# Optimization experiments

Measured on AMD Instinct MI355X. Metric: run time of the kernel, lower is better.

The kernel has to match this reference:

```python
import jax, jax.numpy as jnp
import numpy as np

D_MODEL = 512
NUM_HEADS = 8
D_K = D_MODEL // NUM_HEADS


def setup_inputs() -> dict:
    key = jax.random.key(0)
    ks = jax.random.split(key, 11)
    B, S = 2, 4096
    std = max(0.02, min((1.0 / D_MODEL) ** 0.5, 0.5))
    xavier = (6.0 / (D_MODEL + D_MODEL)) ** 0.5
    return {
        "Q": jax.random.normal(ks[0], (B, S, D_MODEL), jnp.float32),
        "K": jax.random.normal(ks[1], (B, S, D_MODEL), jnp.float32),
        "V": jax.random.normal(ks[2], (B, S, D_MODEL), jnp.float32),
        # torch Linear convention: weight [out, in], y = x @ W.T + b
        "Wq": std * jax.random.truncated_normal(ks[3], -2.0, 2.0, (D_MODEL, D_MODEL), jnp.float32),
        "bq": jnp.zeros((D_MODEL,), jnp.float32),
        "Wk": std * jax.random.truncated_normal(ks[4], -2.0, 2.0, (D_MODEL, D_MODEL), jnp.float32),
        "bk": jnp.zeros((D_MODEL,), jnp.float32),
        "Wv": std * jax.random.truncated_normal(ks[5], -2.0, 2.0, (D_MODEL, D_MODEL), jnp.float32),
        "bv": jnp.zeros((D_MODEL,), jnp.float32),
        "Wo": jax.random.uniform(ks[6], (D_MODEL, D_MODEL), jnp.float32, -xavier, xavier),
        "bo": jnp.zeros((D_MODEL,), jnp.float32),
    }


def _split_heads(x):
    B, S, _ = x.shape
    return x.reshape(B, S, NUM_HEADS, D_K).transpose(0, 2, 1, 3)  # [B,H,S,dk]


def reference(Q, K, V, Wq, bq, Wk, bk, Wv, bv, Wo, bo):
    B, S, _ = Q.shape
    q = _split_heads(Q @ Wq.T + bq)
    k = _split_heads(K @ Wk.T + bk)
    v = _split_heads(V @ Wv.T + bv)
    scores = jnp.einsum("bhqd,bhkd->bhqk", q, k) / (D_K ** 0.5)  # [B,H,S,S]
    causal = jnp.tril(jnp.ones((S, S), bool))  # mask=True path
    scores = jnp.where(causal[None, None], scores, jnp.float32(-1e9))
    attn = jax.nn.softmax(scores, axis=-1)
    out = jnp.einsum("bhqk,bhkd->bhqd", attn, v)
    out = out.transpose(0, 2, 1, 3).reshape(B, S, D_MODEL)
    return out @ Wo.T + bo, attn
```

## Files before the change

kernel.cpp:

```cpp
#include <hip/hip_runtime.h>
#include <stdint.h>

#define B_  2
#define H_  8
#define S_  4096
#define DM_ 512
#define DK_ 64
#define BH_ (B_*H_)

using f32x4 = __attribute__((ext_vector_type(4))) float;
using s16x8 = __attribute__((ext_vector_type(8))) short;
using u16x4 = __attribute__((ext_vector_type(4))) unsigned short;
using u16x8 = __attribute__((ext_vector_type(8))) unsigned short;

__device__ __forceinline__ unsigned short f2bf(float f) {
    unsigned int u = __float_as_uint(f);
    u += 0x7FFFu + ((u >> 16) & 1u);
    return (unsigned short)(u >> 16);
}
__device__ __forceinline__ float bf2f(unsigned short h) {
    return __uint_as_float(((unsigned int)h) << 16);
}

__global__ __launch_bounds__(256) void convert_split(const float* __restrict__ in,
        unsigned short* __restrict__ hi, unsigned short* __restrict__ lo, int n4)
{
    for (int i = blockIdx.x*256 + threadIdx.x; i < n4; i += gridDim.x*256) {
        float4 v = ((const float4*)in)[i];
        float s4[4] = {v.x, v.y, v.z, v.w};
        u16x4 h, l;
#pragma unroll
        for (int j = 0; j < 4; ++j) {
            unsigned short hh = f2bf(s4[j]);
            h[j] = hh; l[j] = f2bf(s4[j] - bf2f(hh));
        }
        ((u16x4*)hi)[i] = h;
        ((u16x4*)lo)[i] = l;
    }
}

__global__ __launch_bounds__(256) void convert_hi(const float* __restrict__ in,
        unsigned short* __restrict__ hi, int n4)
{
    for (int i = blockIdx.x*256 + threadIdx.x; i < n4; i += gridDim.x*256) {
        float4 v = ((const float4*)in)[i];
        u16x4 h;
        h[0] = f2bf(v.x); h[1] = f2bf(v.y); h[2] = f2bf(v.z); h[3] = f2bf(v.w);
        ((u16x4*)hi)[i] = h;
    }
}

template<int MODE>
__global__ __launch_bounds__(256) void proj_kernel(
        const unsigned short* __restrict__ Xh, const unsigned short* __restrict__ Xl,
        const unsigned short* __restrict__ Wh, const unsigned short* __restrict__ Wl,
        const float* __restrict__ bias, unsigned short* __restrict__ Y, float scale)
{
    __shared__ __align__(16) unsigned short xh[64*72], xl[64*72];
    __shared__ __align__(16) unsigned short wh[64*72], wl[64*72];
    const int tid  = threadIdx.x;
    const int wave = tid >> 6, lane = tid & 63, lq = lane >> 4, lr = lane & 15;
    const int m0 = blockIdx.x * 64, n0 = blockIdx.y * 64;

    f32x4 acc[4] = {{0.f,0.f,0.f,0.f},{0.f,0.f,0.f,0.f},
                    {0.f,0.f,0.f,0.f},{0.f,0.f,0.f,0.f}};

    for (int kk = 0; kk < 8; ++kk) {
        __syncthreads();
#pragma unroll
        for (int p = 0; p < 2; ++p) {
            int idx = tid + p*256;
            int row = idx >> 3, seg = idx & 7;
            size_t xoff = (size_t)(m0+row)*DM_ + kk*64 + seg*8;
            size_t woff = (size_t)(n0+row)*DM_ + kk*64 + seg*8;
            *(u16x8*)&xh[row*72 + seg*8] = *(const u16x8*)&Xh[xoff];
            *(u16x8*)&xl[row*72 + seg*8] = *(const u16x8*)&Xl[xoff];
            *(u16x8*)&wh[row*72 + seg*8] = *(const u16x8*)&Wh[woff];
            *(u16x8*)&wl[row*72 + seg*8] = *(const u16x8*)&Wl[woff];
        }
        __syncthreads();
        const int ar = wave*16 + lr;
        s16x8 ah0 = *(const s16x8*)&xh[ar*72 +  0 + lq*8];
        s16x8 ah1 = *(const s16x8*)&xh[ar*72 + 32 + lq*8];
        s16x8 al0 = *(const s16x8*)&xl[ar*72 +  0 + lq*8];
        s16x8 al1 = *(const s16x8*)&xl[ar*72 + 32 + lq*8];
#pragma unroll
        for (int nt = 0; nt < 4; ++nt) {
            int br = nt*16 + lr;
            s16x8 bh0 = *(const s16x8*)&wh[br*72 +  0 + lq*8];
            s16x8 bh1 = *(const s16x8*)&wh[br*72 + 32 + lq*8];
            s16x8 bl0 = *(const s16x8*)&wl[br*72 +  0 + lq*8];
            s16x8 bl1 = *(const s16x8*)&wl[br*72 + 32 + lq*8];
            acc[nt] = __builtin_amdgcn_mfma_f32_16x16x32_bf16(ah0, bh0, acc[nt], 0, 0, 0);
            acc[nt] = __builtin_amdgcn_mfma_f32_16x16x32_bf16(ah0, bl0, acc[nt], 0, 0, 0);
            acc[nt] = __builtin_amdgcn_mfma_f32_16x16x32_bf16(al0, bh0, acc[nt], 0, 0, 0);
            acc[nt] = __builtin_amdgcn_mfma_f32_16x16x32_bf16(ah1, bh1, acc[nt], 0, 0, 0);
            acc[nt] = __builtin_amdgcn_mfma_f32_16x16x32_bf16(ah1, bl1, acc[nt], 0, 0, 0);
            acc[nt] = __builtin_amdgcn_mfma_f32_16x16x32_bf16(al1, bh1, acc[nt], 0, 0, 0);
        }
    }
#pragma unroll
    for (int nt = 0; nt < 4; ++nt)
#pragma unroll
        for (int r = 0; r < 4; ++r) {
            int m = m0 + wave*16 + lq*4 + r;
            int n = n0 + nt*16 + lr;
            float v = (acc[nt][r] + bias[n]) * scale;
            int b = m >> 12, s = m & 4095;
            int h = n >> 6,  d = n & 63;
            size_t addr;
            if (MODE == 0) addr = ((size_t)((b*H_ + h)*S_ + s))*DK_ + d;
            else           addr = ((size_t)((b*H_ + h)*DK_ + d))*S_ + s;
            Y[addr] = f2bf(v);
        }
}

__global__ __launch_bounds__(256) void stats_kernel(
        const unsigned short* __restrict__ qb, const unsigned short* __restrict__ kb,
        float* __restrict__ lsum)
{
    __shared__ __align__(16) unsigned short qs[64*72], ks[64*72];
    const int tid  = threadIdx.x;
    const int wave = tid >> 6, lane = tid & 63, lq = lane >> 4, lr = lane & 15;
    const int bh = blockIdx.y;
    const int s0 = blockIdx.x * 64;

#pragma unroll
    for (int p = 0; p < 2; ++p) {
        int idx = tid + p*256;
        int row = idx >> 3, seg = idx & 7;
        *(s16x8*)&qs[row*72 + seg*8] =
            *(const s16x8*)&qb[((size_t)bh*S_ + s0 + row)*DK_ + seg*8];
    }
    __syncthreads();
    const int ar = wave*16 + lr;
    s16x8 aq0 = *(const s16x8*)&qs[ar*72 +  0 + lq*8];
    s16x8 aq1 = *(const s16x8*)&qs[ar*72 + 32 + lq*8];

    float lacc[4] = {0.f, 0.f, 0.f, 0.f};
    const int jtmax = blockIdx.x;
    for (int jt = 0; jt <= jtmax; ++jt) {
        __syncthreads();
#pragma unroll
        for (int p = 0; p < 2; ++p) {
            int idx = tid + p*256;
            int row = idx >> 3, seg = idx & 7;
            *(s16x8*)&ks[row*72 + seg*8] =
                *(const s16x8*)&kb[((size_t)bh*S_ + jt*64 + row)*DK_ + seg*8];
        }
        __syncthreads();
#pragma unroll
        for (int nt = 0; nt < 4; ++nt) {
            int br = nt*16 + lr;
            s16x8 b0 = *(const s16x8*)&ks[br*72 +  0 + lq*8];
            s16x8 b1 = *(const s16x8*)&ks[br*72 + 32 + lq*8];
            f32x4 sc = {0.f,0.f,0.f,0.f};
            sc = __builtin_amdgcn_mfma_f32_16x16x32_bf16(aq0, b0, sc, 0, 0, 0);
            sc = __builtin_amdgcn_mfma_f32_16x16x32_bf16(aq1, b1, sc, 0, 0, 0);
            int j = jt*64 + nt*16 + lr;
#pragma unroll
            for (int r = 0; r < 4; ++r) {
                int sq = s0 + wave*16 + lq*4 + r;
                lacc[r] += (j <= sq) ? __expf(sc[r] - 16.f) : 0.f;
            }
        }
    }
#pragma unroll
    for (int r = 0; r < 4; ++r) {
        float v = lacc[r];
        for (int off = 1; off < 16; off <<= 1) v += __shfl_xor(v, off, 64);
        if (lr == 0) lsum[(size_t)bh*S_ + s0 + wave*16 + lq*4 + r] = v;
    }
}

__global__ __launch_bounds__(256) void attn_kernel(
        const unsigned short* __restrict__ qb, const unsigned short* __restrict__ kb,
        const unsigned short* __restrict__ vtb, const float* __restrict__ lsum,
        float* __restrict__ attn, unsigned short* __restrict__ oacc)
{
    __shared__ __align__(16) unsigned short qs[64*72], ks[64*72], vs[64*72];
    __shared__ __align__(16) unsigned short ps[4][16*72];
    __shared__ float invl[64];
    const int tid  = threadIdx.x;
    const int wave = tid >> 6, lane = tid & 63, lq = lane >> 4, lr = lane & 15;
    const int bh = blockIdx.y;
    const int s0 = blockIdx.x * 64;

#pragma unroll
    for (int p = 0; p < 2; ++p) {
        int idx = tid + p*256;
        int row = idx >> 3, seg = idx & 7;
        *(s16x8*)&qs[row*72 + seg*8] =
            *(const s16x8*)&qb[((size_t)bh*S_ + s0 + row)*DK_ + seg*8];
    }
    if (tid < 64) invl[tid] = 1.0f / lsum[(size_t)bh*S_ + s0 + tid];
    __syncthreads();
    const int ar = wave*16 + lr;
    s16x8 aq0 = *(const s16x8*)&qs[ar*72 +  0 + lq*8];
    s16x8 aq1 = *(const s16x8*)&qs[ar*72 + 32 + lq*8];
    float il[4];
#pragma unroll
    for (int r = 0; r < 4; ++r) il[r] = invl[wave*16 + lq*4 + r];

    f32x4 O[4] = {{0.f,0.f,0.f,0.f},{0.f,0.f,0.f,0.f},
                  {0.f,0.f,0.f,0.f},{0.f,0.f,0.f,0.f}};
    const int jtcomp = blockIdx.x;

    for (int jt = 0; jt < S_/64; ++jt) {
        if (jt <= jtcomp) {
            __syncthreads();
#pragma unroll
            for (int p = 0; p < 2; ++p) {
                int idx = tid + p*256;
                int row = idx >> 3, seg = idx & 7;
                *(s16x8*)&ks[row*72 + seg*8] =
                    *(const s16x8*)&kb[((size_t)bh*S_ + jt*64 + row)*DK_ + seg*8];
                *(s16x8*)&vs[row*72 + seg*8] =
                    *(const s16x8*)&vtb[((size_t)bh*DK_ + row)*S_ + jt*64 + seg*8];
            }
            __syncthreads();
            float a_all[4][4];
#pragma unroll
            for (int nt = 0; nt < 4; ++nt) {
                int br = nt*16 + lr;
                s16x8 b0 = *(const s16x8*)&ks[br*72 +  0 + lq*8];
                s16x8 b1 = *(const s16x8*)&ks[br*72 + 32 + lq*8];
                f32x4 sc = {0.f,0.f,0.f,0.f};
                sc = __builtin_amdgcn_mfma_f32_16x16x32_bf16(aq0, b0, sc, 0, 0, 0);
                sc = __builtin_amdgcn_mfma_f32_16x16x32_bf16(aq1, b1, sc, 0, 0, 0);
                int j = jt*64 + nt*16 + lr;
#pragma unroll
                for (int r = 0; r < 4; ++r) {
                    int sq = s0 + wave*16 + lq*4 + r;
                    float p = (j <= sq) ? __expf(sc[r] - 16.f) : 0.f;
                    float a = p * il[r];
                    a_all[nt][r] = a;
                    ps[wave][(lq*4 + r)*72 + nt*16 + lr] = f2bf(a);
                }
            }
            asm volatile("s_waitcnt lgkmcnt(0)" ::: "memory");
            __builtin_amdgcn_sched_barrier(0);
            s16x8 ap0 = *(const s16x8*)&ps[wave][lr*72 +  0 + lq*8];
            s16x8 ap1 = *(const s16x8*)&ps[wave][lr*72 + 32 + lq*8];
#pragma unroll
            for (int nt = 0; nt < 4; ++nt) {
                s16x8 bv0 = *(const s16x8*)&vs[(nt*16 + lr)*72 +  0 + lq*8];
                s16x8 bv1 = *(const s16x8*)&vs[(nt*16 + lr)*72 + 32 + lq*8];
                O[nt] = __builtin_amdgcn_mfma_f32_16x16x32_bf16(ap0, bv0, O[nt], 0, 0, 0);
                O[nt] = __builtin_amdgcn_mfma_f32_16x16x32_bf16(ap1, bv1, O[nt], 0, 0, 0);
            }
#pragma unroll
            for (int nt = 0; nt < 4; ++nt)
#pragma unroll
                for (int r = 0; r < 4; ++r) {
                    int sq = s0 + wave*16 + lq*4 + r;
                    attn[((size_t)bh*S_ + sq)*S_ + jt*64 + nt*16 + lr] = a_all[nt][r];
                }
        } else {
#pragma unroll
            for (int p = 0; p < 4; ++p) {
                int idx = tid + p*256;
                int row = idx >> 4, c4 = idx & 15;
                float4 z = {0.f, 0.f, 0.f, 0.f};
                *(float4*)&attn[((size_t)bh*S_ + s0 + row)*S_ + jt*64 + c4*4] = z;
            }
        }
    }
    const int b = bh >> 3, h = bh & 7;
#pragma unroll
    for (int nt = 0; nt < 4; ++nt)
#pragma unroll
        for (int r = 0; r < 4; ++r) {
            int s = s0 + wave*16 + lq*4 + r;
            oacc[((size_t)(b*S_ + s))*DM_ + h*DK_ + nt*16 + lr] = f2bf(O[nt][r]);
        }
}

__global__ __launch_bounds__(256) void outproj_kernel(
        const unsigned short* __restrict__ Xin, const unsigned short* __restrict__ Woh,
        const float* __restrict__ bias, float* __restrict__ out)
{
    __shared__ __align__(16) unsigned short xs[64*72], wsm[64*72];
    const int tid  = threadIdx.x;
    const int wave = tid >> 6, lane = tid & 63, lq = lane >> 4, lr = lane & 15;
    const int m0 = blockIdx.x * 64, n0 = blockIdx.y * 64;

    f32x4 acc[4] = {{0.f,0.f,0.f,0.f},{0.f,0.f,0.f,0.f},
                    {0.f,0.f,0.f,0.f},{0.f,0.f,0.f,0.f}};

    for (int kk = 0; kk < 8; ++kk) {
        __syncthreads();
#pragma unroll
        for (int p = 0; p < 2; ++p) {
            int idx = tid + p*256;
            int row = idx >> 3, seg = idx & 7;
            *(s16x8*)&xs [row*72 + seg*8] =
                *(const s16x8*)&Xin[(size_t)(m0+row)*DM_ + kk*64 + seg*8];
            *(s16x8*)&wsm[row*72 + seg*8] =
                *(const s16x8*)&Woh[(size_t)(n0+row)*DM_ + kk*64 + seg*8];
        }
        __syncthreads();
        const int ar = wave*16 + lr;
        s16x8 a0 = *(const s16x8*)&xs[ar*72 +  0 + lq*8];
        s16x8 a1 = *(const s16x8*)&xs[ar*72 + 32 + lq*8];
#pragma unroll
        for (int nt = 0; nt < 4; ++nt) {
            int br = nt*16 + lr;
            s16x8 b0 = *(const s16x8*)&wsm[br*72 +  0 + lq*8];
            s16x8 b1 = *(const s16x8*)&wsm[br*72 + 32 + lq*8];
            acc[nt] = __builtin_amdgcn_mfma_f32_16x16x32_bf16(a0, b0, acc[nt], 0, 0, 0);
            acc[nt] = __builtin_amdgcn_mfma_f32_16x16x32_bf16(a1, b1, acc[nt], 0, 0, 0);
        }
    }
#pragma unroll
    for (int nt = 0; nt < 4; ++nt)
#pragma unroll
        for (int r = 0; r < 4; ++r) {
            int m = m0 + wave*16 + lq*4 + r;
            int n = n0 + nt*16 + lr;
            out[(size_t)m*DM_ + n] = acc[nt][r] + bias[n];
        }
}

extern "C" void kernel_launch(void* const* d_in, const int* in_sizes, int n_in,
                              void* d_out, int out_size, void* d_ws, size_t ws_size,
                              hipStream_t stream)
{
    const float* Q  = (const float*)d_in[0];
    const float* K  = (const float*)d_in[1];
    const float* V  = (const float*)d_in[2];
    const float* Wq = (const float*)d_in[3];  const float* bq = (const float*)d_in[4];
    const float* Wk = (const float*)d_in[5];  const float* bk = (const float*)d_in[6];
    const float* Wv = (const float*)d_in[7];  const float* bv = (const float*)d_in[8];
    const float* Wo = (const float*)d_in[9];  const float* bo = (const float*)d_in[10];

    char* ws = (char*)d_ws;
    const size_t QKV_BYTES = (size_t)BH_ * S_ * DK_ * sizeof(unsigned short);
    const size_t W_BYTES   = (size_t)DM_ * DM_ * sizeof(unsigned short);
    unsigned short* qbf  = (unsigned short*)(ws);
    unsigned short* kbf  = (unsigned short*)(ws + QKV_BYTES);
    unsigned short* vtb  = (unsigned short*)(ws + 2*QKV_BYTES);
    float*          lsum = (float*)(ws + 3*QKV_BYTES);
    unsigned short* oacc = (unsigned short*)(ws + 3*QKV_BYTES + (size_t)BH_*S_*sizeof(float));
    char* p = ws + 4*QKV_BYTES + (size_t)BH_*S_*sizeof(float);
    unsigned short* xh  = (unsigned short*)(p);               p += QKV_BYTES;
    unsigned short* xl  = (unsigned short*)(p);               p += QKV_BYTES;
    unsigned short* wqh = (unsigned short*)(p);               p += W_BYTES;
    unsigned short* wql = (unsigned short*)(p);               p += W_BYTES;
    unsigned short* wkh = (unsigned short*)(p);               p += W_BYTES;
    unsigned short* wkl = (unsigned short*)(p);               p += W_BYTES;
    unsigned short* wvh = (unsigned short*)(p);               p += W_BYTES;
    unsigned short* wvl = (unsigned short*)(p);               p += W_BYTES;
    unsigned short* woh = (unsigned short*)(p);               p += W_BYTES;

    float* out0 = (float*)d_out;
    float* attn = out0 + (size_t)B_ * S_ * DM_;

    dim3 blk(256);
    const int n4x = B_*S_*DM_/4;
    const int n4w = DM_*DM_/4;
    auto cgrid = [](int n4) { int g = (n4 + 255) / 256; return g > 2048 ? 2048 : g; };

    convert_split<<<cgrid(n4w), blk, 0, stream>>>(Wq, wqh, wql, n4w);
    convert_split<<<cgrid(n4w), blk, 0, stream>>>(Wk, wkh, wkl, n4w);
    convert_split<<<cgrid(n4w), blk, 0, stream>>>(Wv, wvh, wvl, n4w);
    convert_hi   <<<cgrid(n4w), blk, 0, stream>>>(Wo, woh, n4w);

    convert_split<<<cgrid(n4x), blk, 0, stream>>>(Q, xh, xl, n4x);
    proj_kernel<0><<<dim3(128, 8), blk, 0, stream>>>(xh, xl, wqh, wql, bq, qbf, 0.125f);
    convert_split<<<cgrid(n4x), blk, 0, stream>>>(K, xh, xl, n4x);
    proj_kernel<0><<<dim3(128, 8), blk, 0, stream>>>(xh, xl, wkh, wkl, bk, kbf, 1.0f);
    convert_split<<<cgrid(n4x), blk, 0, stream>>>(V, xh, xl, n4x);
    proj_kernel<1><<<dim3(128, 8), blk, 0, stream>>>(xh, xl, wvh, wvl, bv, vtb, 1.0f);

    stats_kernel  <<<dim3(64, 16), blk, 0, stream>>>(qbf, kbf, lsum);
    attn_kernel   <<<dim3(64, 16), blk, 0, stream>>>(qbf, kbf, vtb, lsum, attn, oacc);
    outproj_kernel<<<dim3(128, 8), blk, 0, stream>>>(oacc, woh, bo, out0);
}
```

Before: 1.387 ms.

## Pair causal query tiles per block, stage transposed V stores, nontemporal attn writes

The stats and attention kernels now have each block handle two query tiles, bx and 63-bx. This balances the triangular causal work across blocks and halves the grid. The V-projection epilogue stages its tile in shared memory so the transposed output is written with coalesced 16-byte stores instead of scattered 2-byte ones. The large attention-probability matrix writes, both values and zeros, use nontemporal stores to avoid polluting the cache. The risk is fewer blocks (512) for the available compute units.

New measurement: 1.358 ms. -2.1%, faster.

```diff
diff --git a/kernel.cpp b/kernel.cpp
--- a/kernel.cpp
+++ b/kernel.cpp
@@ -99,20 +99,36 @@
             acc[nt] = __builtin_amdgcn_mfma_f32_16x16x32_bf16(al1, bh1, acc[nt], 0, 0, 0);
         }
     }
-#pragma unroll
-    for (int nt = 0; nt < 4; ++nt)
-#pragma unroll
-        for (int r = 0; r < 4; ++r) {
-            int m = m0 + wave*16 + lq*4 + r;
-            int n = n0 + nt*16 + lr;
-            float v = (acc[nt][r] + bias[n]) * scale;
-            int b = m >> 12, s = m & 4095;
-            int h = n >> 6,  d = n & 63;
-            size_t addr;
-            if (MODE == 0) addr = ((size_t)((b*H_ + h)*S_ + s))*DK_ + d;
-            else           addr = ((size_t)((b*H_ + h)*DK_ + d))*S_ + s;
-            Y[addr] = f2bf(v);
-        }
+    if (MODE == 0) {
+#pragma unroll
+        for (int nt = 0; nt < 4; ++nt)
+#pragma unroll
+            for (int r = 0; r < 4; ++r) {
+                int m = m0 + wave*16 + lq*4 + r;
+                int n = n0 + nt*16 + lr;
+                float v = (acc[nt][r] + bias[n]) * scale;
+                int b = m >> 12, s = m & 4095;
+                int h = n >> 6,  d = n & 63;
+                Y[((size_t)((b*H_ + h)*S_ + s))*DK_ + d] = f2bf(v);
+            }
+    } else {
+        __syncthreads();
+#pragma unroll
+        for (int nt = 0; nt < 4; ++nt)
+#pragma unroll
+            for (int r = 0; r < 4; ++r) {
+                int ml = wave*16 + lq*4 + r;
+                int nl = nt*16 + lr;
+                float v = (acc[nt][r] + bias[n0 + nl]) * scale;
+                xh[nl*72 + ml] = f2bf(v);
+            }
+        __syncthreads();
+        const int b = m0 >> 12, sbase = m0 & 4095, h = n0 >> 6;
+        const int row = tid >> 2, segb = (tid & 3) * 16;
+        size_t base = ((size_t)((b*H_ + h)*DK_ + row))*S_ + sbase + segb;
+        *(u16x8*)&Y[base]     = *(const u16x8*)&xh[row*72 + segb];
+        *(u16x8*)&Y[base + 8] = *(const u16x8*)&xh[row*72 + segb + 8];
+    }
 }
 
 __global__ __launch_bounds__(256) void stats_kernel(
@@ -123,91 +139,26 @@
     const int tid  = threadIdx.x;
     const int wave = tid >> 6, lane = tid & 63, lq = lane >> 4, lr = lane & 15;
     const int bh = blockIdx.y;
-    const int s0 = blockIdx.x * 64;
-
-#pragma unroll
-    for (int p = 0; p < 2; ++p) {
-        int idx = tid + p*256;
-        int row = idx >> 3, seg = idx & 7;
-        *(s16x8*)&qs[row*72 + seg*8] =
-            *(const s16x8*)&qb[((size_t)bh*S_ + s0 + row)*DK_ + seg*8];
-    }
-    __syncthreads();
-    const int ar = wave*16 + lr;
-    s16x8 aq0 = *(const s16x8*)&qs[ar*72 +  0 + lq*8];
-    s16x8 aq1 = *(const s16x8*)&qs[ar*72 + 32 + lq*8];
-
-    float lacc[4] = {0.f, 0.f, 0.f, 0.f};
-    const int jtmax = blockIdx.x;
-    for (int jt = 0; jt <= jtmax; ++jt) {
+
+#pragma unroll 1
+    for (int half = 0; half < 2; ++half) {
+        const int bx = half ? (63 - blockIdx.x) : blockIdx.x;
+        const int s0 = bx * 64;
         __syncthreads();
 #pragma unroll
         for (int p = 0; p < 2; ++p) {
             int idx = tid + p*256;
             int row = idx >> 3, seg = idx & 7;
-            *(s16x8*)&ks[row*72 + seg*8] =
-                *(const s16x8*)&kb[((size_t)bh*S_ + jt*64 + row)*DK_ + seg*8];
-        }
-        __syncthreads();
-#pragma unroll
-        for (int nt = 0; nt < 4; ++nt) {
-            int br = nt*16 + lr;
-            s16x8 b0 = *(const s16x8*)&ks[br*72 +  0 + lq*8];
-            s16x8 b1 = *(const s16x8*)&ks[br*72 + 32 + lq*8];
-            f32x4 sc = {0.f,0.f,0.f,0.f};
-            sc = __builtin_amdgcn_mfma_f32_16x16x32_bf16(aq0, b0, sc, 0, 0, 0);
-            sc = __builtin_amdgcn_mfma_f32_16x16x32_bf16(aq1, b1, sc, 0, 0, 0);
-            int j = jt*64 + nt*16 + lr;
-#pragma unroll
-            for (int r = 0; r < 4; ++r) {
-                int sq = s0 + wave*16 + lq*4 + r;
-                lacc[r] += (j <= sq) ? __expf(sc[r] - 16.f) : 0.f;
-            }
-        }
-    }
-#pragma unroll
-    for (int r = 0; r < 4; ++r) {
-        float v = lacc[r];
-        for (int off = 1; off < 16; off <<= 1) v += __shfl_xor(v, off, 64);
-        if (lr == 0) lsum[(size_t)bh*S_ + s0 + wave*16 + lq*4 + r] = v;
-    }
-}
-
-__global__ __launch_bounds__(256) void attn_kernel(
-        const unsigned short* __restrict__ qb, const unsigned short* __restrict__ kb,
-        const unsigned short* __restrict__ vtb, const float* __restrict__ lsum,
-        float* __restrict__ attn, unsigned short* __restrict__ oacc)
-{
-    __shared__ __align__(16) unsigned short qs[64*72], ks[64*72], vs[64*72];
-    __shared__ __align__(16) unsigned short ps[4][16*72];
-    __shared__ float invl[64];
-    const int tid  = threadIdx.x;
-    const int wave = tid >> 6, lane = tid & 63, lq = lane >> 4, lr = lane & 15;
-    const int bh = blockIdx.y;
-    const int s0 = blockIdx.x * 64;
-
-#pragma unroll
-    for (int p = 0; p < 2; ++p) {
-        int idx = tid + p*256;
-        int row = idx >> 3, seg = idx & 7;
-        *(s16x8*)&qs[row*72 + seg*8] =
-            *(const s16x8*)&qb[((size_t)bh*S_ + s0 + row)*DK_ + seg*8];
-    }
-    if (tid < 64) invl[tid] = 1.0f / lsum[(size_t)bh*S_ + s0 + tid];
-    __syncthreads();
-    const int ar = wave*16 + lr;
-    s16x8 aq0 = *(const s16x8*)&qs[ar*72 +  0 + lq*8];
-    s16x8 aq1 = *(const s16x8*)&qs[ar*72 + 32 + lq*8];
-    float il[4];
-#pragma unroll
-    for (int r = 0; r < 4; ++r) il[r] = invl[wave*16 + lq*4 + r];
-
-    f32x4 O[4] = {{0.f,0.f,0.f,0.f},{0.f,0.f,0.f,0.f},
-                  {0.f,0.f,0.f,0.f},{0.f,0.f,0.f,0.f}};
-    const int jtcomp = blockIdx.x;
-
-    for (int jt = 0; jt < S_/64; ++jt) {
-        if (jt <= jtcomp) {
+            *(s16x8*)&qs[row*72 + seg*8] =
+                *(const s16x8*)&qb[((size_t)bh*S_ + s0 + row)*DK_ + seg*8];
+        }
+        __syncthreads();
+        const int ar = wave*16 + lr;
+        s16x8 aq0 = *(const s16x8*)&qs[ar*72 +  0 + lq*8];
+        s16x8 aq1 = *(const s16x8*)&qs[ar*72 + 32 + lq*8];
+
+        float lacc[4] = {0.f, 0.f, 0.f, 0.f};
+        for (int jt = 0; jt <= bx; ++jt) {
             __syncthreads();
 #pragma unroll
             for (int p = 0; p < 2; ++p) {
@@ -215,11 +166,8 @@
                 int row = idx >> 3, seg = idx & 7;
                 *(s16x8*)&ks[row*72 + seg*8] =
                     *(const s16x8*)&kb[((size_t)bh*S_ + jt*64 + row)*DK_ + seg*8];
-                *(s16x8*)&vs[row*72 + seg*8] =
-                    *(const s16x8*)&vtb[((size_t)bh*DK_ + row)*S_ + jt*64 + seg*8];
             }
             __syncthreads();
-            float a_all[4][4];
 #pragma unroll
             for (int nt = 0; nt < 4; ++nt) {
                 int br = nt*16 + lr;
@@ -232,48 +180,126 @@
 #pragma unroll
                 for (int r = 0; r < 4; ++r) {
                     int sq = s0 + wave*16 + lq*4 + r;
-                    float p = (j <= sq) ? __expf(sc[r] - 16.f) : 0.f;
-                    float a = p * il[r];
-                    a_all[nt][r] = a;
-                    ps[wave][(lq*4 + r)*72 + nt*16 + lr] = f2bf(a);
+                    lacc[r] += (j <= sq) ? __expf(sc[r] - 16.f) : 0.f;
                 }
             }
-            asm volatile("s_waitcnt lgkmcnt(0)" ::: "memory");
-            __builtin_amdgcn_sched_barrier(0);
-            s16x8 ap0 = *(const s16x8*)&ps[wave][lr*72 +  0 + lq*8];
-            s16x8 ap1 = *(const s16x8*)&ps[wave][lr*72 + 32 + lq*8];
-#pragma unroll
-            for (int nt = 0; nt < 4; ++nt) {
-                s16x8 bv0 = *(const s16x8*)&vs[(nt*16 + lr)*72 +  0 + lq*8];
-                s16x8 bv1 = *(const s16x8*)&vs[(nt*16 + lr)*72 + 32 + lq*8];
-                O[nt] = __builtin_amdgcn_mfma_f32_16x16x32_bf16(ap0, bv0, O[nt], 0, 0, 0);
-                O[nt] = __builtin_amdgcn_mfma_f32_16x16x32_bf16(ap1, bv1, O[nt], 0, 0, 0);
-            }
-#pragma unroll
-            for (int nt = 0; nt < 4; ++nt)
-#pragma unroll
-                for (int r = 0; r < 4; ++r) {
-                    int sq = s0 + wave*16 + lq*4 + r;
-                    attn[((size_t)bh*S_ + sq)*S_ + jt*64 + nt*16 + lr] = a_all[nt][r];
+        }
+#pragma unroll
+        for (int r = 0; r < 4; ++r) {
+            float v = lacc[r];
+            for (int off = 1; off < 16; off <<= 1) v += __shfl_xor(v, off, 64);
+            if (lr == 0) lsum[(size_t)bh*S_ + s0 + wave*16 + lq*4 + r] = v;
+        }
+    }
+}
+
+__global__ __launch_bounds__(256) void attn_kernel(
+        const unsigned short* __restrict__ qb, const unsigned short* __restrict__ kb,
+        const unsigned short* __restrict__ vtb, const float* __restrict__ lsum,
+        float* __restrict__ attn, unsigned short* __restrict__ oacc)
+{
+    __shared__ __align__(16) unsigned short qs[64*72], ks[64*72], vs[64*72];
+    __shared__ __align__(16) unsigned short ps[4][16*72];
+    __shared__ float invl[64];
+    const int tid  = threadIdx.x;
+    const int wave = tid >> 6, lane = tid & 63, lq = lane >> 4, lr = lane & 15;
+    const int bh = blockIdx.y;
+
+#pragma unroll 1
+    for (int half = 0; half < 2; ++half) {
+        const int bx = half ? (63 - blockIdx.x) : blockIdx.x;
+        const int s0 = bx * 64;
+        __syncthreads();
+#pragma unroll
+        for (int p = 0; p < 2; ++p) {
+            int idx = tid + p*256;
+            int row = idx >> 3, seg = idx & 7;
+            *(s16x8*)&qs[row*72 + seg*8] =
+                *(const s16x8*)&qb[((size_t)bh*S_ + s0 + row)*DK_ + seg*8];
+        }
+        if (tid < 64) invl[tid] = 1.0f / lsum[(size_t)bh*S_ + s0 + tid];
+        __syncthreads();
+        const int ar = wave*16 + lr;
+        s16x8 aq0 = *(const s16x8*)&qs[ar*72 +  0 + lq*8];
+        s16x8 aq1 = *(const s16x8*)&qs[ar*72 + 32 + lq*8];
+        float il[4];
+#pragma unroll
+        for (int r = 0; r < 4; ++r) il[r] = invl[wave*16 + lq*4 + r];
+
+        f32x4 O[4] = {{0.f,0.f,0.f,0.f},{0.f,0.f,0.f,0.f},
+                      {0.f,0.f,0.f,0.f},{0.f,0.f,0.f,0.f}};
+
+        for (int jt = 0; jt < S_/64; ++jt) {
+            if (jt <= bx) {
+                __syncthreads();
+#pragma unroll
+                for (int p = 0; p < 2; ++p) {
+                    int idx = tid + p*256;
+                    int row = idx >> 3, seg = idx & 7;
+                    *(s16x8*)&ks[row*72 + seg*8] =
+                        *(const s16x8*)&kb[((size_t)bh*S_ + jt*64 + row)*DK_ + seg*8];
+                    *(s16x8*)&vs[row*72 + seg*8] =
+                        *(const s16x8*)&vtb[((size_t)bh*DK_ + row)*S_ + jt*64 + seg*8];
                 }
-        } else {
-#pragma unroll
-            for (int p = 0; p < 4; ++p) {
-                int idx = tid + p*256;
-                int row = idx >> 4, c4 = idx & 15;
-                float4 z = {0.f, 0.f, 0.f, 0.f};
-                *(float4*)&attn[((size_t)bh*S_ + s0 + row)*S_ + jt*64 + c4*4] = z;
-            }
-        }
-    }
-    const int b = bh >> 3, h = bh & 7;
-#pragma unroll
-    for (int nt = 0; nt < 4; ++nt)
-#pragma unroll
-        for (int r = 0; r < 4; ++r) {
-            int s = s0 + wave*16 + lq*4 + r;
-            oacc[((size_t)(b*S_ + s))*DM_ + h*DK_ + nt*16 + lr] = f2bf(O[nt][r]);
-        }
+                __syncthreads();
+                float a_all[4][4];
+#pragma unroll
+                for (int nt = 0; nt < 4; ++nt) {
+                    int br = nt*16 + lr;
+                    s16x8 b0 = *(const s16x8*)&ks[br*72 +  0 + lq*8];
+                    s16x8 b1 = *(const s16x8*)&ks[br*72 + 32 + lq*8];
+                    f32x4 sc = {0.f,0.f,0.f,0.f};
+                    sc = __builtin_amdgcn_mfma_f32_16x16x32_bf16(aq0, b0, sc, 0, 0, 0);
+                    sc = __builtin_amdgcn_mfma_f32_16x16x32_bf16(aq1, b1, sc, 0, 0, 0);
+                    int j = jt*64 + nt*16 + lr;
+#pragma unroll
+                    for (int r = 0; r < 4; ++r) {
+                        int sq = s0 + wave*16 + lq*4 + r;
+                        float p = (j <= sq) ? __expf(sc[r] - 16.f) : 0.f;
+                        float a = p * il[r];
+                        a_all[nt][r] = a;
+                        ps[wave][(lq*4 + r)*72 + nt*16 + lr] = f2bf(a);
+                    }
+                }
+                asm volatile("s_waitcnt lgkmcnt(0)" ::: "memory");
+                __builtin_amdgcn_sched_barrier(0);
+                s16x8 ap0 = *(const s16x8*)&ps[wave][lr*72 +  0 + lq*8];
+                s16x8 ap1 = *(const s16x8*)&ps[wave][lr*72 + 32 + lq*8];
+#pragma unroll
+                for (int nt = 0; nt < 4; ++nt) {
+                    s16x8 bv0 = *(const s16x8*)&vs[(nt*16 + lr)*72 +  0 + lq*8];
+                    s16x8 bv1 = *(const s16x8*)&vs[(nt*16 + lr)*72 + 32 + lq*8];
+                    O[nt] = __builtin_amdgcn_mfma_f32_16x16x32_bf16(ap0, bv0, O[nt], 0, 0, 0);
+                    O[nt] = __builtin_amdgcn_mfma_f32_16x16x32_bf16(ap1, bv1, O[nt], 0, 0, 0);
+                }
+#pragma unroll
+                for (int nt = 0; nt < 4; ++nt)
+#pragma unroll
+                    for (int r = 0; r < 4; ++r) {
+                        int sq = s0 + wave*16 + lq*4 + r;
+                        __builtin_nontemporal_store(a_all[nt][r],
+                            &attn[((size_t)bh*S_ + sq)*S_ + jt*64 + nt*16 + lr]);
+                    }
+            } else {
+#pragma unroll
+                for (int p = 0; p < 4; ++p) {
+                    int idx = tid + p*256;
+                    int row = idx >> 4, c4 = idx & 15;
+                    f32x4 z = {0.f, 0.f, 0.f, 0.f};
+                    __builtin_nontemporal_store(z,
+                        (f32x4*)&attn[((size_t)bh*S_ + s0 + row)*S_ + jt*64 + c4*4]);
+                }
+            }
+        }
+        const int b = bh >> 3, h = bh & 7;
+#pragma unroll
+        for (int nt = 0; nt < 4; ++nt)
+#pragma unroll
+            for (int r = 0; r < 4; ++r) {
+                int s = s0 + wave*16 + lq*4 + r;
+                oacc[((size_t)(b*S_ + s))*DM_ + h*DK_ + nt*16 + lr] = f2bf(O[nt][r]);
+            }
+    }
 }
 
 __global__ __launch_bounds__(256) void outproj_kernel(
@@ -373,7 +399,7 @@
     convert_split<<<cgrid(n4x), blk, 0, stream>>>(V, xh, xl, n4x);
     proj_kernel<1><<<dim3(128, 8), blk, 0, stream>>>(xh, xl, wvh, wvl, bv, vtb, 1.0f);
 
-    stats_kernel  <<<dim3(64, 16), blk, 0, stream>>>(qbf, kbf, lsum);
-    attn_kernel   <<<dim3(64, 16), blk, 0, stream>>>(qbf, kbf, vtb, lsum, attn, oacc);
+    stats_kernel  <<<dim3(32, 16), blk, 0, stream>>>(qbf, kbf, lsum);
+    attn_kernel   <<<dim3(32, 16), blk, 0, stream>>>(qbf, kbf, vtb, lsum, attn, oacc);
     outproj_kernel<<<dim3(128, 8), blk, 0, stream>>>(oacc, woh, bo, out0);
 }
```
